# Kernel tuning notes

Measured on AMD Instinct MI355X. Metric: run time of the kernel, lower is better.

The kernel has to match this reference:

```python
import jax, jax.numpy as jnp
import numpy as np

HID = 128

def setup_inputs() -> dict:
    key = jax.random.key(0)
    ks = jax.random.split(key, 16)
    T, N, E = 32, 10000, 160000
    features = jax.random.normal(ks[0], (T, N, 1), dtype=jnp.float32)
    src = jax.random.randint(ks[1], (E,), 0, N)
    dst = jax.random.randint(ks[2], (E,), 0, N)
    s = 0.1
    # GraphConv params (stored as [in,out] so y = x @ W + b)
    W1 = jax.random.normal(ks[3], (1, 32), dtype=jnp.float32) * s
    b1 = jnp.zeros((32,), jnp.float32)
    W2 = jax.random.normal(ks[4], (32, HID), dtype=jnp.float32) * s
    b2 = jnp.zeros((HID,), jnp.float32)
    # attention-pool gate nn.Linear(128,1)
    gate_w = jax.random.normal(ks[5], (HID, 1), dtype=jnp.float32) * s
    gate_b = jnp.zeros((1,), jnp.float32)
    # GRU params, PyTorch layout: [3H, in], gate order (r, z, n)
    W_ih = jax.random.normal(ks[6], (3 * HID, HID), dtype=jnp.float32) * s
    W_hh = jax.random.normal(ks[7], (3 * HID, HID), dtype=jnp.float32) * s
    b_ih = jnp.zeros((3 * HID,), jnp.float32)
    b_hh = jnp.zeros((3 * HID,), jnp.float32)
    # dense layers ([in,out])
    d1_w = jax.random.normal(ks[8], (HID, 16), dtype=jnp.float32) * s
    d1_b = jnp.zeros((16,), jnp.float32)
    d2_w = jax.random.normal(ks[9], (16, 4), dtype=jnp.float32) * s
    d2_b = jnp.zeros((4,), jnp.float32)
    return {"features": features, "src": src, "dst": dst,
            "W1": W1, "b1": b1, "W2": W2, "b2": b2,
            "gate_w": gate_w, "gate_b": gate_b,
            "W_ih": W_ih, "W_hh": W_hh, "b_ih": b_ih, "b_hh": b_hh,
            "d1_w": d1_w, "d1_b": d1_b, "d2_w": d2_w, "d2_b": d2_b}


def reference(features, src, dst, W1, b1, W2, b2, gate_w, gate_b,
              W_ih, W_hh, b_ih, b_hh, d1_w, d1_b, d2_w, d2_b):
    T, N, _ = features.shape
    E = src.shape[0]
    ones = jnp.ones((E,), features.dtype)
    out_deg = jnp.clip(jax.ops.segment_sum(ones, src, num_segments=N), 1.0)
    in_deg = jnp.clip(jax.ops.segment_sum(ones, dst, num_segments=N), 1.0)
    norm_out = out_deg ** -0.5  # DGL GraphConv norm='both' (src side)
    norm_in = in_deg ** -0.5    # dst side

    def gconv(h, W, b):
        # h: [N, F] -> scale by src norm, gather, scatter-add to dst, scale, linear, SiLU
        msg = (h * norm_out[:, None])[src]               # [E, F]
        agg = jax.ops.segment_sum(msg, dst, num_segments=N)  # [N, F]
        return jax.nn.silu((agg * norm_in[:, None]) @ W + b)

    def per_frame(f):  # f: [N,1]
        return gconv(gconv(f, W1, b1), W2, b2)  # [N, HID]

    h = jax.vmap(per_frame)(features)  # [T, N, HID]

    # GlobalAttentionPooling: softmax over nodes of gate_nn(h)
    gate = h @ gate_w + gate_b                 # [T, N, 1]
    alpha = jax.nn.softmax(gate, axis=1)
    pooled = jnp.sum(alpha * h, axis=1)        # [T, HID]

    # single-layer GRU, batch=1, take final hidden state
    def gru_step(hprev, x):
        gi = x @ W_ih.T + b_ih
        gh = hprev @ W_hh.T + b_hh
        i_r, i_z, i_n = jnp.split(gi, 3)
        h_r, h_z, h_n = jnp.split(gh, 3)
        r = jax.nn.sigmoid(i_r + h_r)
        z = jax.nn.sigmoid(i_z + h_z)
        n = jnp.tanh(i_n + r * h_n)
        hnew = (1.0 - z) * n + z * hprev
        return hnew, None

    h0 = jnp.zeros((HID,), features.dtype)
    hT, _ = jax.lax.scan(gru_step, h0, pooled)

    out = jax.nn.silu(hT @ d1_w + d1_b)
    out = jax.nn.silu(out @ d2_w + d2_b)
    return jax.nn.sigmoid(out).reshape(1, 4)
```

## Files before the change

kernel.cpp:

```cpp
#include <hip/hip_runtime.h>
#include <stdint.h>

#define T_FRAMES 32
#define NNODES 10000
#define NEDGES 160000
#define HID 128
#define LGX 32

#define H1_SCALE 512.0f
#define H1_INV   (1.0f/512.0f)

typedef short v8s __attribute__((ext_vector_type(8)));
typedef float v4f __attribute__((ext_vector_type(4)));

static __device__ __forceinline__ ushort f2bf(float f){
  uint32_t u = __float_as_uint(f);
  u += 0x7FFFu + ((u >> 16) & 1u);
  return (ushort)(u >> 16);
}
static __device__ __forceinline__ float fsigm(float x){
  return __fdividef(1.0f, 1.0f + __expf(-x));
}
static __device__ __forceinline__ float fsilu(float x){
  return x * fsigm(x);
}
static __device__ __forceinline__ float ftanh(float x){
  return 2.0f * fsigm(2.0f * x) - 1.0f;
}


__global__ void k_degree(const int* __restrict__ src, const int* __restrict__ dst,
                         int* cnt_out, int* cnt_in, int E){
  int e = blockIdx.x*blockDim.x + threadIdx.x;
  if (e < E){
    atomicAdd(&cnt_out[src[e]], 1);
    atomicAdd(&cnt_in[dst[e]], 1);
  }
}

__global__ void __launch_bounds__(1024) k_scan(const int* __restrict__ cnt_in,
                                               const int* __restrict__ cnt_out,
                                               int* row_ptr, int* cursor,
                                               float* norm_out, float* norm_in, int N){
  __shared__ int wsum[16];
  __shared__ int wexcl[16];
  int tid = threadIdx.x, lane = tid & 63, wid = tid >> 6;
  const int C = 10;
  int base = tid * C;
  int v[C];
  int s = 0;
  #pragma unroll
  for (int i = 0; i < C; ++i){
    int idx = base + i;
    int c = (idx < N) ? cnt_in[idx] : 0;
    v[i] = c;
    s += c;
    if (idx < N){
      norm_in[idx]  = rsqrtf((float)max(c, 1));
      norm_out[idx] = rsqrtf((float)max(cnt_out[idx], 1));
    }
  }
  int x = s;
  #pragma unroll
  for (int off = 1; off < 64; off <<= 1){
    int y = __shfl_up(x, off);
    if (lane >= off) x += y;
  }
  if (lane == 63) wsum[wid] = x;
  __syncthreads();
  if (tid == 0){
    int run = 0;
    #pragma unroll
    for (int w = 0; w < 16; ++w){ int t = wsum[w]; wexcl[w] = run; run += t; }
    row_ptr[N] = run;
  }
  __syncthreads();
  int run = wexcl[wid] + x - s;
  #pragma unroll
  for (int i = 0; i < C; ++i){
    int idx = base + i;
    if (idx < N){ row_ptr[idx] = run; cursor[idx] = run; run += v[i]; }
  }
}

__global__ void k_fill(const int* __restrict__ src, const int* __restrict__ dst,
                       int* cursor, int* es, int E){
  int e = blockIdx.x*blockDim.x + threadIdx.x;
  if (e < E){
    int p = atomicAdd(&cursor[dst[e]], 1);
    es[p] = src[e];
  }
}


__global__ void __launch_bounds__(256) k_fnT(const float* __restrict__ feat,
                                             const float* __restrict__ norm_o,
                                             float* __restrict__ fnT,
                                             const float* __restrict__ W2,
                                             ushort* __restrict__ W2F, int N){
  __shared__ float sm[32][65];
  int n0 = blockIdx.x*64;
  int tid = threadIdx.x;
  for (int idx = tid; idx < 2048; idx += 256){
    int t = idx >> 6, i = idx & 63;
    int n = n0 + i;
    sm[t][i] = (n < N) ? feat[(size_t)t*N + n] : 0.f;
  }
  __syncthreads();
  for (int idx = tid; idx < 2048; idx += 256){
    int i = idx >> 5, t = idx & 31;
    int n = n0 + i;
    if (n < N) fnT[(size_t)n*32 + t] = sm[t][i] * norm_o[n];
  }
  if (blockIdx.x < 16){
    int t2 = blockIdx.x*256 + tid;
    int j = t2 & 7, l = (t2 >> 3) & 63, i = t2 >> 9;
    int g = l >> 4, n = l & 15;
    W2F[t2] = f2bf(W2[(g*8 + j)*128 + i*16 + n]);
  }
}


__global__ void __launch_bounds__(256) k_gconv1_nm(
    const float* __restrict__ fnT, const int* __restrict__ row_ptr,
    const int* __restrict__ es, const float* __restrict__ norm_in,
    const float* __restrict__ norm_out,
    const float* __restrict__ W1, const float* __restrict__ b1,
    uchar* __restrict__ h1s, int N){
  __shared__ float w1s[32], b1s[32];
  int tid = threadIdx.x;
  if (tid < 32){ w1s[tid] = W1[tid]; b1s[tid] = b1[tid]; }
  __syncthreads();
  int n = blockIdx.x*4 + (tid >> 6);
  int lane = tid & 63;
  int ep = lane >> 5, t = lane & 31;
  int s = row_ptr[n], d = row_ptr[n+1];
  float acc = 0.f;
  int e = s + ep;
  for (; e + 6 < d; e += 8){
    float v0 = fnT[(size_t)es[e]  *32 + t];
    float v1 = fnT[(size_t)es[e+2]*32 + t];
    float v2 = fnT[(size_t)es[e+4]*32 + t];
    float v3 = fnT[(size_t)es[e+6]*32 + t];
    acc += v0 + v1 + v2 + v3;
  }
  for (; e < d; e += 2)
    acc += fnT[(size_t)es[e]*32 + t];
  acc += __shfl_xor(acc, 32);
  float x1 = acc * norm_in[n];
  float x1p = __shfl(x1, lane >> 1);
  float no = norm_out[n];
  int j0 = (lane & 1) * 16;
  float hv[16];
  #pragma unroll
  for (int q = 0; q < 16; ++q)
    hv[q] = fsilu(fmaf(x1p, w1s[j0+q], b1s[j0+q])) * no;
  uint b[4] = {0u, 0u, 0u, 0u};
  #pragma unroll
  for (int q = 0; q < 16; ++q){
    float t8 = fminf(fmaxf(fmaf(hv[q], H1_SCALE, 128.5f), 0.f), 255.f);
    b[q >> 2] |= ((uint)(int)t8) << ((q & 3) * 8);
  }
  *(uint4*)(h1s + (size_t)n*1024 + lane*16) = make_uint4(b[0], b[1], b[2], b[3]);
}


__global__ void __launch_bounds__(256) k_gconv2_nm(
    const uchar* __restrict__ h1s, const int* __restrict__ row_ptr,
    const int* __restrict__ es, const float* __restrict__ norm_in,
    ushort* __restrict__ x2, int N){
  int tid = threadIdx.x;
  int n = blockIdx.x*4 + (tid >> 6);
  int lane = tid & 63;
  int s = row_ptr[n], d = row_ptr[n+1];
  float acc[16];
  #pragma unroll
  for (int i = 0; i < 16; ++i) acc[i] = 0.f;

  #define ACCB(v) do { \
    acc[0]  += (float)((v).x & 0xffu);         acc[1]  += (float)(((v).x >> 8) & 0xffu); \
    acc[2]  += (float)(((v).x >> 16) & 0xffu); acc[3]  += (float)((v).x >> 24); \
    acc[4]  += (float)((v).y & 0xffu);         acc[5]  += (float)(((v).y >> 8) & 0xffu); \
    acc[6]  += (float)(((v).y >> 16) & 0xffu); acc[7]  += (float)((v).y >> 24); \
    acc[8]  += (float)((v).z & 0xffu);         acc[9]  += (float)(((v).z >> 8) & 0xffu); \
    acc[10] += (float)(((v).z >> 16) & 0xffu); acc[11] += (float)((v).z >> 24); \
    acc[12] += (float)((v).w & 0xffu);         acc[13] += (float)(((v).w >> 8) & 0xffu); \
    acc[14] += (float)(((v).w >> 16) & 0xffu); acc[15] += (float)((v).w >> 24); \
  } while(0)

  int e = s;
  for (; e + 7 < d; e += 8){
    uint4 w0 = *((const uint4*)(h1s + (size_t)es[e]  *1024) + lane);
    uint4 w1 = *((const uint4*)(h1s + (size_t)es[e+1]*1024) + lane);
    uint4 w2 = *((const uint4*)(h1s + (size_t)es[e+2]*1024) + lane);
    uint4 w3 = *((const uint4*)(h1s + (size_t)es[e+3]*1024) + lane);
    uint4 w4 = *((const uint4*)(h1s + (size_t)es[e+4]*1024) + lane);
    uint4 w5 = *((const uint4*)(h1s + (size_t)es[e+5]*1024) + lane);
    uint4 w6 = *((const uint4*)(h1s + (size_t)es[e+6]*1024) + lane);
    uint4 w7 = *((const uint4*)(h1s + (size_t)es[e+7]*1024) + lane);
    ACCB(w0); ACCB(w1); ACCB(w2); ACCB(w3);
    ACCB(w4); ACCB(w5); ACCB(w6); ACCB(w7);
  }
  for (; e < d; ++e){
    uint4 w0 = *((const uint4*)(h1s + (size_t)es[e]*1024) + lane);
    ACCB(w0);
  }
  #undef ACCB

  float ni = norm_in[n];
  float corr = -128.0f * (float)(d - s);
  float sc = H1_INV * ni;
  uint w[8];
  #pragma unroll
  for (int q = 0; q < 8; ++q){
    float v0 = (acc[2*q]   + corr) * sc;
    float v1 = (acc[2*q+1] + corr) * sc;
    w[q] = (uint)f2bf(v0) | ((uint)f2bf(v1) << 16);
  }
  uint4* dp = (uint4*)(x2 + (size_t)n*1024 + lane*16);
  dp[0] = make_uint4(w[0], w[1], w[2], w[3]);
  dp[1] = make_uint4(w[4], w[5], w[6], w[7]);
}


__global__ void __launch_bounds__(256) k_linear_fused(
    const ushort* __restrict__ x2, const ushort* __restrict__ W2F,
    const float* __restrict__ b2, const float* __restrict__ gate_w,
    const float* __restrict__ gate_b,
    float* __restrict__ Zp, float* __restrict__ pooled_un, int N){
  __shared__ float pool_s[128];
  __shared__ float z_s[4];
  int t = blockIdx.y;
  int tid = threadIdx.x;
  int wave = tid >> 6, lane = tid & 63;
  int g = lane >> 4, n = lane & 15;
  if (tid < 128) pool_s[tid] = 0.f;
  if (tid < 4) z_s[tid] = 0.f;
  __syncthreads();

  const v8s* W2Fv = (const v8s*)W2F;
  v8s bfrag[8];
  #pragma unroll
  for (int i = 0; i < 8; ++i) bfrag[i] = W2Fv[i*64 + lane];
  float gw8[8], bv8[8];
  #pragma unroll
  for (int i = 0; i < 8; ++i){ gw8[i] = gate_w[i*16 + n]; bv8[i] = b2[i*16 + n]; }
  float gb = gate_b[0];

  float cs_acc[8];
  #pragma unroll
  for (int i = 0; i < 8; ++i) cs_acc[i] = 0.f;
  float z_acc = 0.f;

  int wslot = blockIdx.x*4 + wave;
  for (int tile = wslot; tile*16 < N; tile += 128){
    int nb = tile*16;
    const v8s* ap = (const v8s*)(x2 + (size_t)(nb + n)*1024 + t*32);
    v8s a = ap[g];
    v4f acc[8];
    #pragma unroll
    for (int i = 0; i < 8; ++i) acc[i] = (v4f){bv8[i], bv8[i], bv8[i], bv8[i]};
    #pragma unroll
    for (int i = 0; i < 8; ++i)
      acc[i] = __builtin_amdgcn_mfma_f32_16x16x32_bf16(a, bfrag[i], acc[i], 0, 0, 0);

    float hs[8][4];
    #pragma unroll
    for (int i = 0; i < 8; ++i){
      #pragma unroll
      for (int r = 0; r < 4; ++r) hs[i][r] = fsilu(acc[i][r]);
    }
    float gp[4] = {0.f, 0.f, 0.f, 0.f};
    #pragma unroll
    for (int i = 0; i < 8; ++i){
      #pragma unroll
      for (int r = 0; r < 4; ++r) gp[r] += hs[i][r] * gw8[i];
    }
    #pragma unroll
    for (int m = 1; m < 16; m <<= 1){
      #pragma unroll
      for (int r = 0; r < 4; ++r) gp[r] += __shfl_xor(gp[r], m);
    }
    float wn[4];
    #pragma unroll
    for (int r = 0; r < 4; ++r) wn[r] = __expf(gp[r] + gb);
    if (n == 0) z_acc += wn[0] + wn[1] + wn[2] + wn[3];
    #pragma unroll
    for (int i = 0; i < 8; ++i){
      #pragma unroll
      for (int r = 0; r < 4; ++r) cs_acc[i] += hs[i][r] * wn[r];
    }
  }

  z_acc += __shfl_xor(z_acc, 16);
  z_acc += __shfl_xor(z_acc, 32);
  if (lane == 0) z_s[wave] = z_acc;
  #pragma unroll
  for (int i = 0; i < 8; ++i){
    cs_acc[i] += __shfl_xor(cs_acc[i], 16);
    cs_acc[i] += __shfl_xor(cs_acc[i], 32);
  }
  if (lane < 16){
    #pragma unroll
    for (int i = 0; i < 8; ++i) atomicAdd(&pool_s[i*16 + lane], cs_acc[i]);
  }
  __syncthreads();
  if (tid == 0)
    Zp[(size_t)t*LGX + blockIdx.x] = z_s[0] + z_s[1] + z_s[2] + z_s[3];
  if (tid < 128) atomicAdd(&pooled_un[(size_t)t*HID + tid], pool_s[tid]);
}


__global__ void __launch_bounds__(384) k_gi(const float* __restrict__ pooled_un,
                                            const float* __restrict__ Zp,
                                            const float* __restrict__ W_ih,
                                            const float* __restrict__ b_ih,
                                            float* __restrict__ gi_all){
  __shared__ float ps[HID];
  __shared__ float zred[6];
  int t = blockIdx.x, tid = threadIdx.x;
  int lane = tid & 63, wid = tid >> 6;
  float zs = 0.f;
  for (int i = tid; i < LGX; i += 384) zs += Zp[(size_t)t*LGX + i];
  #pragma unroll
  for (int m = 32; m; m >>= 1) zs += __shfl_xor(zs, m);
  if (lane == 0) zred[wid] = zs;
  __syncthreads();
  float invZ = __fdividef(1.0f, zred[0]+zred[1]+zred[2]+zred[3]+zred[4]+zred[5]);
  if (tid < HID) ps[tid] = pooled_un[(size_t)t*HID + tid] * invZ;
  __syncthreads();
  float acc = b_ih[tid];
  const float4* wr = (const float4*)(W_ih + (size_t)tid*HID);
  const float4* p4 = (const float4*)ps;
  #pragma unroll
  for (int q = 0; q < HID/4; ++q){
    float4 wv = wr[q], pv = p4[q];
    acc = fmaf(wv.x, pv.x, acc);
    acc = fmaf(wv.y, pv.y, acc);
    acc = fmaf(wv.z, pv.z, acc);
    acc = fmaf(wv.w, pv.w, acc);
  }
  gi_all[t*384 + tid] = acc;
}

__global__ void __launch_bounds__(768) k_gru(
    const float* __restrict__ gi_all, const float* __restrict__ W_hh,
    const float* __restrict__ b_hh,
    const float* __restrict__ d1_w, const float* __restrict__ d1_b,
    const float* __restrict__ d2_w, const float* __restrict__ d2_b,
    float* __restrict__ out){
  __shared__ float gi_s[T_FRAMES*3*HID];
  __shared__ float ps[2*384];
  __shared__ float h_s[HID];
  __shared__ float o1[16];
  int tid = threadIdx.x;
  int half = (tid >= 384) ? 1 : 0;
  int o = tid - half*384;

  for (int i = tid; i < T_FRAMES*3*HID; i += 768) gi_s[i] = gi_all[i];

  const float4* wr = (const float4*)(W_hh + (size_t)o*HID + half*64);
  #define LDW(i) float4 W##i = wr[i];
  LDW(0) LDW(1) LDW(2) LDW(3) LDW(4) LDW(5) LDW(6) LDW(7)
  LDW(8) LDW(9) LDW(10) LDW(11) LDW(12) LDW(13) LDW(14) LDW(15)
  #undef LDW
  float bh2 = half ? 0.f : b_hh[o];

  if (tid < HID) h_s[tid] = 0.f;
  __syncthreads();

  for (int t = 0; t < T_FRAMES; ++t){
    const float4* p4 = (const float4*)h_s + half*16;
    float acc = bh2;
    #define STEP(i) { float4 pv = p4[i]; \
      acc = fmaf(W##i.x, pv.x, acc); acc = fmaf(W##i.y, pv.y, acc); \
      acc = fmaf(W##i.z, pv.z, acc); acc = fmaf(W##i.w, pv.w, acc); }
    STEP(0) STEP(1) STEP(2) STEP(3) STEP(4) STEP(5) STEP(6) STEP(7)
    STEP(8) STEP(9) STEP(10) STEP(11) STEP(12) STEP(13) STEP(14) STEP(15)
    #undef STEP
    ps[tid] = acc;
    __syncthreads();
    if (tid < HID){
      const float* gi = gi_s + t*384;
      float ghr = ps[tid]       + ps[384+tid];
      float ghz = ps[128+tid]   + ps[512+tid];
      float ghn = ps[256+tid]   + ps[640+tid];
      float r  = fsigm(gi[tid]       + ghr);
      float z  = fsigm(gi[HID+tid]   + ghz);
      float nn = ftanh(gi[2*HID+tid] + r*ghn);
      h_s[tid] = (1.f - z)*nn + z*h_s[tid];
    }
    __syncthreads();
  }
  if (tid < 16){
    float acc = d1_b[tid];
    #pragma unroll 4
    for (int j = 0; j < HID; ++j) acc = fmaf(h_s[j], d1_w[j*16 + tid], acc);
    o1[tid] = fsilu(acc);
  }
  __syncthreads();
  if (tid < 4){
    float acc = d2_b[tid];
    #pragma unroll
    for (int j = 0; j < 16; ++j) acc = fmaf(o1[j], d2_w[j*4 + tid], acc);
    out[tid] = fsigm(fsilu(acc));
  }
}


extern "C" void kernel_launch(void* const* d_in, const int* in_sizes, int n_in,
                              void* d_out, int out_size, void* d_ws, size_t ws_size,
                              hipStream_t stream){
  const float* features = (const float*)d_in[0];
  const int*   src      = (const int*)  d_in[1];
  const int*   dst      = (const int*)  d_in[2];
  const float* W1       = (const float*)d_in[3];
  const float* b1       = (const float*)d_in[4];
  const float* W2       = (const float*)d_in[5];
  const float* b2       = (const float*)d_in[6];
  const float* gate_w   = (const float*)d_in[7];
  const float* gate_b   = (const float*)d_in[8];
  const float* W_ih     = (const float*)d_in[9];
  const float* W_hh     = (const float*)d_in[10];
  const float* b_ih     = (const float*)d_in[11];
  const float* b_hh     = (const float*)d_in[12];
  const float* d1_w     = (const float*)d_in[13];
  const float* d1_b     = (const float*)d_in[14];
  const float* d2_w     = (const float*)d_in[15];
  const float* d2_b     = (const float*)d_in[16];
  float* out = (float*)d_out;

  const int N = NNODES, E = NEDGES, T = T_FRAMES;

  char* base = (char*)d_ws;
  size_t off = 0;
  auto alloc = [&](size_t bytes)->void*{
    void* p = base + off;
    off = (off + bytes + 255) & ~(size_t)255;
    return p;
  };
  int*    cnt_out = (int*)   alloc((size_t)N*4);
  int*    cnt_in  = (int*)   alloc((size_t)N*4);
  float*  pooled  = (float*) alloc((size_t)T*HID*4);
  size_t zero_span = off;
  int*    row_ptr = (int*)   alloc((size_t)(N+1)*4);
  int*    cursor  = (int*)   alloc((size_t)N*4);
  float*  norm_o  = (float*) alloc((size_t)N*4);
  float*  norm_i  = (float*) alloc((size_t)N*4);
  int*    es      = (int*)   alloc((size_t)E*4);
  float*  fnT     = (float*) alloc((size_t)N*T*4);
  uchar*  h1s     = (uchar*) alloc((size_t)N*1024);
  ushort* x2      = (ushort*)alloc((size_t)N*T*32*2);
  float*  Zp      = (float*) alloc((size_t)T*LGX*4);
  float*  gi_all  = (float*) alloc((size_t)T*3*HID*4);
  ushort* W2F     = (ushort*)alloc((size_t)8*64*8*2);
  (void)ws_size; (void)in_sizes; (void)n_in; (void)out_size;

  hipMemsetAsync(d_ws, 0, zero_span, stream);

  k_degree<<<(E+255)/256, 256, 0, stream>>>(src, dst, cnt_out, cnt_in, E);
  k_scan  <<<1, 1024, 0, stream>>>(cnt_in, cnt_out, row_ptr, cursor, norm_o, norm_i, N);
  k_fill  <<<(E+255)/256, 256, 0, stream>>>(src, dst, cursor, es, E);

  k_fnT      <<<(N+63)/64, 256, 0, stream>>>(features, norm_o, fnT, W2, W2F, N);
  k_gconv1_nm<<<N/4, 256, 0, stream>>>(fnT, row_ptr, es, norm_i, norm_o, W1, b1, h1s, N);
  k_gconv2_nm<<<N/4, 256, 0, stream>>>(h1s, row_ptr, es, norm_i, x2, N);

  k_linear_fused<<<dim3(LGX, T), 256, 0, stream>>>(x2, W2F, b2, gate_w, gate_b, Zp, pooled, N);

  k_gi <<<T, 384, 0, stream>>>(pooled, Zp, W_ih, b_ih, gi_all);
  k_gru<<<1, 768, 0, stream>>>(gi_all, W_hh, b_hh, d1_w, d1_b, d2_w, d2_b, out);
}
```

Baseline: 178.2 us.

## Fuse small kernels: merge fill with fnT, fold gi into GRU, replace memset

Merges the CSR fill kernel with the feature transpose/normalize and W2 repack kernel into one launch, sharing blocks by index range. Removes the separate k_gi kernel and computes the input projection inside the single-block GRU loop with W_ih held in registers alongside W_hh. Replaces hipMemsetAsync with a small zeroing kernel. This cuts launch count and inter-kernel gaps, but it puts the W_ih matvec on the serial single-block GRU path and doubles per-thread register weights.

```diff
diff --git a/kernel.cpp b/kernel.cpp
--- a/kernel.cpp
+++ b/kernel.cpp
@@ -26,6 +26,12 @@
 }
 static __device__ __forceinline__ float ftanh(float x){
   return 2.0f * fsigm(2.0f * x) - 1.0f;
+}
+
+
+__global__ void k_zero(float4* __restrict__ p, int n4){
+  int i = blockIdx.x*blockDim.x + threadIdx.x;
+  if (i < n4) p[i] = make_float4(0.f, 0.f, 0.f, 0.f);
 }
 
 
@@ -83,37 +89,38 @@
   }
 }
 
-__global__ void k_fill(const int* __restrict__ src, const int* __restrict__ dst,
-                       int* cursor, int* es, int E){
-  int e = blockIdx.x*blockDim.x + threadIdx.x;
+
+__global__ void __launch_bounds__(256) k_fill_fnT(
+    const int* __restrict__ src, const int* __restrict__ dst,
+    int* cursor, int* es, int E,
+    const float* __restrict__ feat, const float* __restrict__ norm_o,
+    float* __restrict__ fnT,
+    const float* __restrict__ W2, ushort* __restrict__ W2F, int N){
+  __shared__ float sm[32][65];
+  int tid = threadIdx.x;
+  int bx = blockIdx.x;
+
+  int e = bx*256 + tid;
   if (e < E){
     int p = atomicAdd(&cursor[dst[e]], 1);
     es[p] = src[e];
   }
-}
-
-
-__global__ void __launch_bounds__(256) k_fnT(const float* __restrict__ feat,
-                                             const float* __restrict__ norm_o,
-                                             float* __restrict__ fnT,
-                                             const float* __restrict__ W2,
-                                             ushort* __restrict__ W2F, int N){
-  __shared__ float sm[32][65];
-  int n0 = blockIdx.x*64;
-  int tid = threadIdx.x;
-  for (int idx = tid; idx < 2048; idx += 256){
-    int t = idx >> 6, i = idx & 63;
-    int n = n0 + i;
-    sm[t][i] = (n < N) ? feat[(size_t)t*N + n] : 0.f;
-  }
-  __syncthreads();
-  for (int idx = tid; idx < 2048; idx += 256){
-    int i = idx >> 5, t = idx & 31;
-    int n = n0 + i;
-    if (n < N) fnT[(size_t)n*32 + t] = sm[t][i] * norm_o[n];
-  }
-  if (blockIdx.x < 16){
-    int t2 = blockIdx.x*256 + tid;
+
+  if (bx < 157){
+    int n0 = bx*64;
+    for (int idx = tid; idx < 2048; idx += 256){
+      int t = idx >> 6, i = idx & 63;
+      int n = n0 + i;
+      sm[t][i] = (n < N) ? feat[(size_t)t*N + n] : 0.f;
+    }
+    __syncthreads();
+    for (int idx = tid; idx < 2048; idx += 256){
+      int i = idx >> 5, t = idx & 31;
+      int n = n0 + i;
+      if (n < N) fnT[(size_t)n*32 + t] = sm[t][i] * norm_o[n];
+    }
+  } else if (bx < 173){
+    int t2 = (bx - 157)*256 + tid;
     int j = t2 & 7, l = (t2 >> 3) & 63, i = t2 >> 9;
     int g = l >> 4, n = l & 15;
     W2F[t2] = f2bf(W2[(g*8 + j)*128 + i*16 + n]);
@@ -311,83 +318,65 @@
 }
 
 
-__global__ void __launch_bounds__(384) k_gi(const float* __restrict__ pooled_un,
-                                            const float* __restrict__ Zp,
-                                            const float* __restrict__ W_ih,
-                                            const float* __restrict__ b_ih,
-                                            float* __restrict__ gi_all){
-  __shared__ float ps[HID];
-  __shared__ float zred[6];
-  int t = blockIdx.x, tid = threadIdx.x;
-  int lane = tid & 63, wid = tid >> 6;
-  float zs = 0.f;
-  for (int i = tid; i < LGX; i += 384) zs += Zp[(size_t)t*LGX + i];
-  #pragma unroll
-  for (int m = 32; m; m >>= 1) zs += __shfl_xor(zs, m);
-  if (lane == 0) zred[wid] = zs;
-  __syncthreads();
-  float invZ = __fdividef(1.0f, zred[0]+zred[1]+zred[2]+zred[3]+zred[4]+zred[5]);
-  if (tid < HID) ps[tid] = pooled_un[(size_t)t*HID + tid] * invZ;
-  __syncthreads();
-  float acc = b_ih[tid];
-  const float4* wr = (const float4*)(W_ih + (size_t)tid*HID);
-  const float4* p4 = (const float4*)ps;
-  #pragma unroll
-  for (int q = 0; q < HID/4; ++q){
-    float4 wv = wr[q], pv = p4[q];
-    acc = fmaf(wv.x, pv.x, acc);
-    acc = fmaf(wv.y, pv.y, acc);
-    acc = fmaf(wv.z, pv.z, acc);
-    acc = fmaf(wv.w, pv.w, acc);
-  }
-  gi_all[t*384 + tid] = acc;
-}
-
-__global__ void __launch_bounds__(768) k_gru(
-    const float* __restrict__ gi_all, const float* __restrict__ W_hh,
-    const float* __restrict__ b_hh,
+__global__ void __launch_bounds__(768, 1) k_gru(
+    const float* __restrict__ pooled_un, const float* __restrict__ Zp,
+    const float* __restrict__ W_ih, const float* __restrict__ b_ih,
+    const float* __restrict__ W_hh, const float* __restrict__ b_hh,
     const float* __restrict__ d1_w, const float* __restrict__ d1_b,
     const float* __restrict__ d2_w, const float* __restrict__ d2_b,
     float* __restrict__ out){
-  __shared__ float gi_s[T_FRAMES*3*HID];
-  __shared__ float ps[2*384];
-  __shared__ float h_s[HID];
+  __shared__ float tmp_i[768], tmp_h[768];
+  __shared__ float ps_cur[HID], h_s[HID];
+  __shared__ float invZ_s[T_FRAMES];
   __shared__ float o1[16];
   int tid = threadIdx.x;
   int half = (tid >= 384) ? 1 : 0;
   int o = tid - half*384;
 
-  for (int i = tid; i < T_FRAMES*3*HID; i += 768) gi_s[i] = gi_all[i];
-
-  const float4* wr = (const float4*)(W_hh + (size_t)o*HID + half*64);
-  #define LDW(i) float4 W##i = wr[i];
+  const float4* wih = (const float4*)(W_ih + (size_t)o*HID + half*64);
+  const float4* whh = (const float4*)(W_hh + (size_t)o*HID + half*64);
+  #define LDW(i) float4 WI##i = wih[i]; float4 WH##i = whh[i];
   LDW(0) LDW(1) LDW(2) LDW(3) LDW(4) LDW(5) LDW(6) LDW(7)
   LDW(8) LDW(9) LDW(10) LDW(11) LDW(12) LDW(13) LDW(14) LDW(15)
   #undef LDW
+  float bi2 = half ? 0.f : b_ih[o];
   float bh2 = half ? 0.f : b_hh[o];
 
+  if (tid < T_FRAMES){
+    float z = 0.f;
+    for (int i = 0; i < LGX; ++i) z += Zp[tid*LGX + i];
+    invZ_s[tid] = __fdividef(1.0f, z);
+  }
   if (tid < HID) h_s[tid] = 0.f;
   __syncthreads();
 
   for (int t = 0; t < T_FRAMES; ++t){
-    const float4* p4 = (const float4*)h_s + half*16;
-    float acc = bh2;
-    #define STEP(i) { float4 pv = p4[i]; \
-      acc = fmaf(W##i.x, pv.x, acc); acc = fmaf(W##i.y, pv.y, acc); \
-      acc = fmaf(W##i.z, pv.z, acc); acc = fmaf(W##i.w, pv.w, acc); }
+    if (tid < HID) ps_cur[tid] = pooled_un[(size_t)t*HID + tid] * invZ_s[t];
+    __syncthreads();
+    const float4* p4 = (const float4*)ps_cur + half*16;
+    const float4* h4 = (const float4*)h_s + half*16;
+    float ai = bi2, ah = bh2;
+    #define STEP(i) { float4 pv = p4[i]; float4 hv = h4[i]; \
+      ai = fmaf(WI##i.x, pv.x, ai); ai = fmaf(WI##i.y, pv.y, ai); \
+      ai = fmaf(WI##i.z, pv.z, ai); ai = fmaf(WI##i.w, pv.w, ai); \
+      ah = fmaf(WH##i.x, hv.x, ah); ah = fmaf(WH##i.y, hv.y, ah); \
+      ah = fmaf(WH##i.z, hv.z, ah); ah = fmaf(WH##i.w, hv.w, ah); }
     STEP(0) STEP(1) STEP(2) STEP(3) STEP(4) STEP(5) STEP(6) STEP(7)
     STEP(8) STEP(9) STEP(10) STEP(11) STEP(12) STEP(13) STEP(14) STEP(15)
     #undef STEP
-    ps[tid] = acc;
+    tmp_i[tid] = ai;
+    tmp_h[tid] = ah;
     __syncthreads();
     if (tid < HID){
-      const float* gi = gi_s + t*384;
-      float ghr = ps[tid]       + ps[384+tid];
-      float ghz = ps[128+tid]   + ps[512+tid];
-      float ghn = ps[256+tid]   + ps[640+tid];
-      float r  = fsigm(gi[tid]       + ghr);
-      float z  = fsigm(gi[HID+tid]   + ghz);
-      float nn = ftanh(gi[2*HID+tid] + r*ghn);
+      float gir = tmp_i[tid]       + tmp_i[384+tid];
+      float giz = tmp_i[128+tid]   + tmp_i[512+tid];
+      float gin = tmp_i[256+tid]   + tmp_i[640+tid];
+      float ghr = tmp_h[tid]       + tmp_h[384+tid];
+      float ghz = tmp_h[128+tid]   + tmp_h[512+tid];
+      float ghn = tmp_h[256+tid]   + tmp_h[640+tid];
+      float r  = fsigm(gir + ghr);
+      float z  = fsigm(giz + ghz);
+      float nn = ftanh(gin + r*ghn);
       h_s[tid] = (1.f - z)*nn + z*h_s[tid];
     }
     __syncthreads();
@@ -452,22 +441,22 @@
   uchar*  h1s     = (uchar*) alloc((size_t)N*1024);
   ushort* x2      = (ushort*)alloc((size_t)N*T*32*2);
   float*  Zp      = (float*) alloc((size_t)T*LGX*4);
-  float*  gi_all  = (float*) alloc((size_t)T*3*HID*4);
   ushort* W2F     = (ushort*)alloc((size_t)8*64*8*2);
   (void)ws_size; (void)in_sizes; (void)n_in; (void)out_size;
 
-  hipMemsetAsync(d_ws, 0, zero_span, stream);
+  int n4 = (int)(zero_span / 16);
+  k_zero  <<<(n4+255)/256, 256, 0, stream>>>((float4*)d_ws, n4);
 
   k_degree<<<(E+255)/256, 256, 0, stream>>>(src, dst, cnt_out, cnt_in, E);
   k_scan  <<<1, 1024, 0, stream>>>(cnt_in, cnt_out, row_ptr, cursor, norm_o, norm_i, N);
-  k_fill  <<<(E+255)/256, 256, 0, stream>>>(src, dst, cursor, es, E);
-
-  k_fnT      <<<(N+63)/64, 256, 0, stream>>>(features, norm_o, fnT, W2, W2F, N);
+  k_fill_fnT<<<(E+255)/256, 256, 0, stream>>>(src, dst, cursor, es, E,
+                                              features, norm_o, fnT, W2, W2F, N);
+
   k_gconv1_nm<<<N/4, 256, 0, stream>>>(fnT, row_ptr, es, norm_i, norm_o, W1, b1, h1s, N);
   k_gconv2_nm<<<N/4, 256, 0, stream>>>(h1s, row_ptr, es, norm_i, x2, N);
 
   k_linear_fused<<<dim3(LGX, T), 256, 0, stream>>>(x2, W2F, b2, gate_w, gate_b, Zp, pooled, N);
 
-  k_gi <<<T, 384, 0, stream>>>(pooled, Zp, W_ih, b_ih, gi_all);
-  k_gru<<<1, 768, 0, stream>>>(gi_all, W_hh, b_hh, d1_w, d1_b, d2_w, d2_b, out);
-}
+  k_gru<<<1, 768, 0, stream>>>(pooled, Zp, W_ih, b_ih, W_hh, b_hh,
+                               d1_w, d1_b, d2_w, d2_b, out);
+}
```

After: 189.8 us. 6.5% more time.
